# Optimization experiments

Hardware: AMD Instinct MI355X
Metric: run time of the kernel (lower is better)

Reference implementation:

```python
import jax, jax.numpy as jnp
import numpy as np

IN_CH = 256
HID = 64
HEADS = 3 * 0 + 4  # num_heads


def setup_inputs() -> dict:
    key = jax.random.key(0)
    ks = jax.random.split(key, 5)
    B, C, H, W = 2, IN_CH, 64, 64
    x = jax.random.normal(ks[0], (B, C, H, W), dtype=jnp.float32)
    # per-head embed conv (kernel 1 -> stored as [heads, 3*HID, C]); kaiming fan_out-ish scale
    w_embed = jax.random.normal(ks[1], (HEADS, 3 * HID, C), dtype=jnp.float32) * np.float32(np.sqrt(2.0 / (3 * HID)))
    b_embed = jnp.zeros((HEADS, 3 * HID), dtype=jnp.float32)
    # output ConvTranspose2d(hidden*heads -> C, kernel 1): weight [hidden*heads, C]
    w_out = jax.random.normal(ks[2], (HEADS * HID, C), dtype=jnp.float32) * np.float32(np.sqrt(2.0 / C))
    b_out = jnp.zeros((C,), dtype=jnp.float32)
    return {"x": x, "w_embed": w_embed, "b_embed": b_embed, "w_out": w_out, "b_out": b_out}


def reference(x, w_embed, b_embed, w_out, b_out):
    B, C, H, W = x.shape
    N = H * W
    nH = w_embed.shape[0]
    D = w_embed.shape[1] // 3
    scale = D ** -0.5
    # 1x1 embed conv per head: [B, nH, 3D, N]
    xf = x.reshape(B, C, N)
    qkv = jnp.einsum('bcn,hdc->bhdn', xf, w_embed) + b_embed[None, :, :, None]
    q, k, v = jnp.split(qkv, 3, axis=2)  # each [B, nH, D, N]
    attn = jnp.einsum('bhci,bhcj->bhij', q, k) * scale  # [B, nH, N, N]
    attn = jax.nn.softmax(attn, axis=-1)
    y = jnp.einsum('bhij,bhcj->bhci', attn, v)  # [B, nH, D, N]
    y = y.reshape(B, nH * D, N)
    # output 1x1 transposed conv (kernel 1 == plain 1x1 projection)
    out = jnp.einsum('bkn,kc->bcn', y, w_out) + b_out[None, :, None]
    out = out.reshape(B, C, H, W)
    return out + x  # residual
```

## Files before the change

kernel.cpp:

```cpp
#include <hip/hip_runtime.h>
#include <hip/hip_bf16.h>

#define NH   4
#define D_   64
#define N_   4096
#define C_   256
#define ME   768
#define QSCALE 0.18033688f

typedef float    f32x4  __attribute__((ext_vector_type(4)));
typedef float    f32x16 __attribute__((ext_vector_type(16)));
typedef _Float16 f16x8  __attribute__((ext_vector_type(8)));
typedef _Float16 f16x4  __attribute__((ext_vector_type(4)));

__global__ __launch_bounds__(256) void prep_kernel(const float* __restrict__ x,
                                                   const float* __restrict__ w_out,
                                                   _Float16* __restrict__ xT,
                                                   _Float16* __restrict__ w_outT) {
    __shared__ float T[64][68];
    const int t = threadIdx.x, bx = blockIdx.x;
    if (bx < 512) {
        const int n0 = (bx & 63) * 64, c0 = ((bx >> 6) & 3) * 64, b = bx >> 8;
        const float* xp = x + ((size_t)b * C_ + c0) * N_ + n0;
        #pragma unroll
        for (int r = 0; r < 4; ++r) {
            int idx = r * 256 + t;
            int c = idx >> 4, ng = (idx & 15) * 4;
            *(f32x4*)&T[c][ng] = *(const f32x4*)(xp + (size_t)c * N_ + ng);
        }
        __syncthreads();
        _Float16* dp = xT + ((size_t)b * N_ + n0) * C_ + c0;
        #pragma unroll
        for (int r = 0; r < 2; ++r) {
            int idx = r * 256 + t;
            int n = idx >> 3, cg = (idx & 7) * 8;
            f16x8 v;
            #pragma unroll
            for (int j = 0; j < 8; ++j) v[j] = (_Float16)T[cg + j][n];
            *(f16x8*)(dp + (size_t)n * C_ + cg) = v;
        }
    } else {
        int tile = bx - 512;
        int tc = tile & 3, tk = tile >> 2;
        #pragma unroll
        for (int r = 0; r < 4; ++r) {
            int idx = r * 256 + t;
            int kl = idx >> 4, cl = (idx & 15) * 4;
            *(f32x4*)&T[kl][cl] = *(const f32x4*)(w_out + (size_t)(tk * 64 + kl) * C_ + tc * 64 + cl);
        }
        __syncthreads();
        #pragma unroll
        for (int r = 0; r < 2; ++r) {
            int idx = r * 256 + t;
            int cl = idx >> 3, kg = (idx & 7) * 8;
            f16x8 v;
            #pragma unroll
            for (int j = 0; j < 8; ++j) v[j] = (_Float16)T[kg + j][cl];
            *(f16x8*)(w_outT + (size_t)(tc * 64 + cl) * C_ + tk * 64 + kg) = v;
        }
    }
}

__global__ __launch_bounds__(256) void qkv_gemm(const _Float16* __restrict__ xT,
                                                const float* __restrict__ w_embed,
                                                const float* __restrict__ b_embed,
                                                _Float16* __restrict__ qT,
                                                _Float16* __restrict__ kT,
                                                _Float16* __restrict__ vB) {
    __shared__ __align__(16) union SM {
        struct { _Float16 A[2][64][40], X[2][64][40]; } s;
        float Os[64][68];
    } sm;
    const int n0 = blockIdx.x * 64, mt = blockIdx.y, b = blockIdx.z;
    const int m0 = mt * 64;
    const int t = threadIdx.x;
    const int lane = t & 63, w = t >> 6, quad = lane >> 4, l16 = lane & 15;
    const int srow = t >> 2, skoff = (t & 3) * 8;
    const int h = mt / 3, r3 = mt - h * 3;
    const float oscale = (r3 == 0) ? QSCALE : 1.0f;
    const float* ap = w_embed + (size_t)(m0 + srow) * C_ + skoff;
    const _Float16* xp = xT + ((size_t)b * N_ + n0 + srow) * C_ + skoff;
    f32x4 a0pre = *(const f32x4*)(ap);
    f32x4 a1pre = *(const f32x4*)(ap + 4);
    f16x8 xpre  = *(const f16x8*)(xp);
    f32x4 acc[4] = {};
    int cur = 0;
    for (int k0 = 0; k0 < C_; k0 += 32, cur ^= 1) {
        {
            f16x8 av = { (_Float16)a0pre[0], (_Float16)a0pre[1], (_Float16)a0pre[2], (_Float16)a0pre[3],
                         (_Float16)a1pre[0], (_Float16)a1pre[1], (_Float16)a1pre[2], (_Float16)a1pre[3] };
            *(f16x8*)&sm.s.A[cur][srow][skoff] = av;
            *(f16x8*)&sm.s.X[cur][srow][skoff] = xpre;
        }
        __syncthreads();
        if (k0 + 32 < C_) {
            a0pre = *(const f32x4*)(ap + k0 + 32);
            a1pre = *(const f32x4*)(ap + k0 + 36);
            xpre  = *(const f16x8*)(xp + k0 + 32);
        }
        f16x8 af = *(const f16x8*)&sm.s.A[cur][w * 16 + l16][quad * 8];
        #pragma unroll
        for (int nb = 0; nb < 4; ++nb) {
            f16x8 bf = *(const f16x8*)&sm.s.X[cur][nb * 16 + l16][quad * 8];
            acc[nb] = __builtin_amdgcn_mfma_f32_16x16x32_f16(af, bf, acc[nb], 0, 0, 0);
        }
    }
    float bias[4];
    #pragma unroll
    for (int rg = 0; rg < 4; ++rg) bias[rg] = b_embed[m0 + w * 16 + quad * 4 + rg];
    __syncthreads();
    #pragma unroll
    for (int nb = 0; nb < 4; ++nb)
        #pragma unroll
        for (int rg = 0; rg < 4; ++rg)
            sm.Os[w * 16 + quad * 4 + rg][nb * 16 + l16] = (acc[nb][rg] + bias[rg]) * oscale;
    __syncthreads();
    const int bh = b * NH + h;
    if (r3 < 2) {
        _Float16* dst = (r3 ? kT : qT) + ((size_t)bh * N_ + n0) * D_;
        #pragma unroll
        for (int r = 0; r < 2; ++r) {
            int idx = r * 256 + t;
            int n = idx >> 3, mg = (idx & 7) * 8;
            f16x8 v;
            #pragma unroll
            for (int j = 0; j < 8; ++j) v[j] = (_Float16)sm.Os[mg + j][n];
            *(f16x8*)(dst + (size_t)n * D_ + mg) = v;
        }
    } else {
        _Float16* dst = vB + (size_t)bh * D_ * N_ + n0;
        #pragma unroll
        for (int r = 0; r < 2; ++r) {
            int idx = r * 256 + t;
            int d = idx >> 3, ng = (idx & 7) * 8;
            f32x4 a = *(const f32x4*)&sm.Os[d][ng];
            f32x4 b2 = *(const f32x4*)&sm.Os[d][ng + 4];
            f16x8 v = { (_Float16)a[0], (_Float16)a[1], (_Float16)a[2], (_Float16)a[3],
                        (_Float16)b2[0], (_Float16)b2[1], (_Float16)b2[2], (_Float16)b2[3] };
            *(f16x8*)(dst + (size_t)d * N_ + ng) = v;
        }
    }
}

__global__ __launch_bounds__(256, 4) void attn_kernel(const _Float16* __restrict__ qT,
                                                      const _Float16* __restrict__ kT,
                                                      const _Float16* __restrict__ vB,
                                                      _Float16* __restrict__ opart,
                                                      float* __restrict__ mpart,
                                                      float* __restrict__ lpart,
                                                      int splog) {
    __shared__ __align__(16) union SM {
        struct { _Float16 K[64][76], V[64][76]; } s;
        _Float16 Os[128][76];
    } sm;
    const int t = threadIdx.x;
    const int nsp = 1 << splog;
    const int qt = blockIdx.x, h = blockIdx.y;
    const int b = blockIdx.z >> splog, s = blockIdx.z & (nsp - 1);
    const int bh = b * NH + h, sbh = s * 8 + bh;
    const _Float16* kp = kT + (size_t)bh * N_ * D_;
    const _Float16* vp = vB + (size_t)bh * D_ * N_;
    const int lane = t & 63, w = t >> 6, l32 = lane & 31, hl = lane >> 5;
    const int srow = t >> 3, scol = (t & 7) * 8;

    const _Float16* qp = qT + ((size_t)bh * N_ + qt * 128 + w * 32 + l32) * D_;
    f16x8 qf[4];
    #pragma unroll
    for (int kc = 0; kc < 4; ++kc) qf[kc] = *(const f16x8*)(qp + kc * 16 + hl * 8);

    f32x16 oacc0 = {}, oacc1 = {};
    float m_run = 0.f, l_run = 0.f;

    const int niter = 64 >> splog;
    const int jt_lo = s * niter, jt_hi = jt_lo + niter;
    f16x8 kpre[2], vpre[2];
    #pragma unroll
    for (int r = 0; r < 2; ++r) {
        int row = srow + r * 32;
        kpre[r] = *(const f16x8*)(kp + (size_t)(jt_lo * 64 + row) * D_ + scol);
        vpre[r] = *(const f16x8*)(vp + (size_t)row * N_ + jt_lo * 64 + scol);
    }

    for (int jt = jt_lo; jt < jt_hi; ++jt) {
        __syncthreads();
        #pragma unroll
        for (int r = 0; r < 2; ++r) {
            int row = srow + r * 32;
            *(f16x8*)&sm.s.K[row][scol] = kpre[r];
            *(f16x8*)&sm.s.V[row][scol] = vpre[r];
        }
        __syncthreads();
        if (jt + 1 < jt_hi) {
            #pragma unroll
            for (int r = 0; r < 2; ++r) {
                int row = srow + r * 32;
                kpre[r] = *(const f16x8*)(kp + (size_t)((jt + 1) * 64 + row) * D_ + scol);
                vpre[r] = *(const f16x8*)(vp + (size_t)row * N_ + (jt + 1) * 64 + scol);
            }
        }
        f32x16 sa0 = {}, sa1 = {};
        #pragma unroll
        for (int kc = 0; kc < 4; ++kc) {
            f16x8 kf0 = *(const f16x8*)&sm.s.K[l32][kc * 16 + hl * 8];
            sa0 = __builtin_amdgcn_mfma_f32_32x32x16_f16(kf0, qf[kc], sa0, 0, 0, 0);
            f16x8 kf1 = *(const f16x8*)&sm.s.K[32 + l32][kc * 16 + hl * 8];
            sa1 = __builtin_amdgcn_mfma_f32_32x32x16_f16(kf1, qf[kc], sa1, 0, 0, 0);
        }
        if (jt == jt_lo) {
            f32x16 mm;
            #pragma unroll
            for (int r = 0; r < 16; ++r) mm[r] = fmaxf(sa0[r], sa1[r]);
            f32x4 m4;
            #pragma unroll
            for (int r = 0; r < 4; ++r)
                m4[r] = fmaxf(fmaxf(mm[r], mm[r + 4]), fmaxf(mm[r + 8], mm[r + 12]));
            float mx = fmaxf(fmaxf(m4[0], m4[1]), fmaxf(m4[2], m4[3]));
            mx = fmaxf(mx, __shfl_xor(mx, 32));
            m_run = mx + 8.0f;
        }
        #pragma unroll
        for (int r = 0; r < 16; ++r) sa0[r] = __builtin_amdgcn_exp2f(sa0[r] - m_run);
        #pragma unroll
        for (int r = 0; r < 16; ++r) sa1[r] = __builtin_amdgcn_exp2f(sa1[r] - m_run);
        f32x16 sv = sa0 + sa1;
        f32x4 s4;
        #pragma unroll
        for (int r = 0; r < 4; ++r) s4[r] = (sv[r] + sv[r + 4]) + (sv[r + 8] + sv[r + 12]);
        float rs = (s4[0] + s4[1]) + (s4[2] + s4[3]);
        rs += __shfl_xor(rs, 32);
        l_run += rs;
        #pragma unroll
        for (int jb = 0; jb < 2; ++jb) {
            const f32x16& sa = jb ? sa1 : sa0;
            union BU { f16x4 v; int d[2]; } bf[4];
            #pragma unroll
            for (int q = 0; q < 8; ++q)
                bf[q >> 1].d[q & 1] =
                    __builtin_bit_cast(int, __builtin_amdgcn_cvt_pkrtz(sa[2 * q], sa[2 * q + 1]));
            #pragma unroll
            for (int c = 0; c < 4; ++c) {
                const int vcol = jb * 32 + c * 8 + hl * 4;
                f16x4 va = *(const f16x4*)&sm.s.V[l32][vcol];
                oacc0 = __builtin_amdgcn_mfma_f32_32x32x8f16(va, bf[c].v, oacc0, 0, 0, 0);
                f16x4 vb = *(const f16x4*)&sm.s.V[32 + l32][vcol];
                oacc1 = __builtin_amdgcn_mfma_f32_32x32x8f16(vb, bf[c].v, oacc1, 0, 0, 0);
            }
        }
    }
    float linv = 1.f / l_run;
    if (hl == 0) {
        mpart[(size_t)sbh * N_ + qt * 128 + w * 32 + l32] = m_run;
        lpart[(size_t)sbh * N_ + qt * 128 + w * 32 + l32] = l_run;
    }
    __syncthreads();
    #pragma unroll
    for (int db = 0; db < 2; ++db) {
        const f32x16& oc = db ? oacc1 : oacc0;
        #pragma unroll
        for (int rq = 0; rq < 4; ++rq) {
            f16x4 pv = { (_Float16)(oc[rq * 4 + 0] * linv), (_Float16)(oc[rq * 4 + 1] * linv),
                         (_Float16)(oc[rq * 4 + 2] * linv), (_Float16)(oc[rq * 4 + 3] * linv) };
            *(f16x4*)&sm.Os[w * 32 + l32][db * 32 + rq * 8 + hl * 4] = pv;
        }
    }
    __syncthreads();
    _Float16* op = opart + ((size_t)sbh * N_ + qt * 128) * D_;
    #pragma unroll
    for (int r = 0; r < 4; ++r) {
        int idx = r * 256 + t;
        int i = idx >> 3, ch = (idx & 7) * 8;
        *(f16x8*)(op + (size_t)i * D_ + ch) = *(const f16x8*)&sm.Os[i][ch];
    }
}

__global__ __launch_bounds__(256) void projc_gemm(const _Float16* __restrict__ opart,
                                                  const float* __restrict__ mpart,
                                                  const float* __restrict__ lpart,
                                                  const _Float16* __restrict__ w_outT,
                                                  const float* __restrict__ b_out,
                                                  const float* __restrict__ x,
                                                  float* __restrict__ out) {
    __shared__ __align__(16) union SMP {
        struct {
            _Float16 Y[16][264];
            union { float W[4][16][4]; _Float16 A[128][40]; } u;
        } p;
        float Os[128][20];
    } sm;
    const int nt = blockIdx.x, chh = blockIdx.y, b = blockIdx.z;
    const int n0 = nt * 16, c0 = chh * 128;
    const int t = threadIdx.x;
    const int lane = t & 63, w = t >> 6, quad = lane >> 4, l16 = lane & 15;

    if (t < 64) {
        const int nl = t & 15, hh = t >> 4;
        const int bh = b * NH + hh;
        float mv[4], lv[4];
        #pragma unroll
        for (int sI = 0; sI < 4; ++sI) {
            mv[sI] = mpart[(size_t)(sI * 8 + bh) * N_ + n0 + nl];
            lv[sI] = lpart[(size_t)(sI * 8 + bh) * N_ + n0 + nl];
        }
        float M = fmaxf(fmaxf(mv[0], mv[1]), fmaxf(mv[2], mv[3]));
        float ws[4], sum = 0.f;
        #pragma unroll
        for (int sI = 0; sI < 4; ++sI) {
            ws[sI] = __builtin_amdgcn_exp2f(mv[sI] - M) * lv[sI];
            sum += ws[sI];
        }
        float inv = 1.f / sum;
        #pragma unroll
        for (int sI = 0; sI < 4; ++sI) sm.p.u.W[hh][nl][sI] = ws[sI] * inv;
    }
    __syncthreads();

    #pragma unroll
    for (int it = 0; it < 2; ++it) {
        int idx = it * 256 + t;
        int n = idx >> 5, kg = (idx & 31) * 8;
        int hh = kg >> 6, d0 = kg & 63;
        const int bh = b * NH + hh;
        const float* Wn = &sm.p.u.W[hh][n][0];
        float accf[8] = {};
        #pragma unroll
        for (int sI = 0; sI < 4; ++sI) {
            f16x8 ov = *(const f16x8*)(opart + ((size_t)(sI * 8 + bh) * N_ + n0 + n) * D_ + d0);
            float wsv = Wn[sI];
            #pragma unroll
            for (int j = 0; j < 8; ++j) accf[j] += wsv * (float)ov[j];
        }
        f16x8 yv;
        #pragma unroll
        for (int j = 0; j < 8; ++j) yv[j] = (_Float16)accf[j];
        *(f16x8*)&sm.p.Y[n][kg] = yv;
    }
    __syncthreads();

    const int srow = t >> 1, skoff = (t & 1) * 16;
    const _Float16* ap = w_outT + (size_t)(c0 + srow) * C_ + skoff;
    f16x8 apre0 = *(const f16x8*)(ap);
    f16x8 apre1 = *(const f16x8*)(ap + 8);
    f32x4 acc[2] = {};
    for (int k0 = 0; k0 < C_; k0 += 32) {
        __syncthreads();
        *(f16x8*)&sm.p.u.A[srow][skoff]     = apre0;
        *(f16x8*)&sm.p.u.A[srow][skoff + 8] = apre1;
        __syncthreads();
        if (k0 + 32 < C_) {
            apre0 = *(const f16x8*)(ap + k0 + 32);
            apre1 = *(const f16x8*)(ap + k0 + 40);
        }
        f16x8 bf = *(const f16x8*)&sm.p.Y[l16][k0 + quad * 8];
        #pragma unroll
        for (int cb = 0; cb < 2; ++cb) {
            f16x8 af = *(const f16x8*)&sm.p.u.A[w * 32 + cb * 16 + l16][quad * 8];
            acc[cb] = __builtin_amdgcn_mfma_f32_16x16x32_f16(af, bf, acc[cb], 0, 0, 0);
        }
    }
    __syncthreads();
    #pragma unroll
    for (int cb = 0; cb < 2; ++cb)
        #pragma unroll
        for (int rg = 0; rg < 4; ++rg)
            sm.Os[w * 32 + cb * 16 + quad * 4 + rg][l16] =
                acc[cb][rg] + b_out[c0 + w * 32 + cb * 16 + quad * 4 + rg];
    __syncthreads();
    const float* xp = x + ((size_t)b * C_ + c0) * N_ + n0;
    float* op = out + ((size_t)b * C_ + c0) * N_ + n0;
    #pragma unroll
    for (int r = 0; r < 2; ++r) {
        int idx = r * 256 + t;
        int c = idx >> 2, ng = (idx & 3) * 4;
        f32x4 v  = *(const f32x4*)&sm.Os[c][ng];
        f32x4 xv = *(const f32x4*)(xp + (size_t)c * N_ + ng);
        f32x4 o  = { v[0] + xv[0], v[1] + xv[1], v[2] + xv[2], v[3] + xv[3] };
        *(f32x4*)(op + (size_t)c * N_ + ng) = o;
    }
}

extern "C" void kernel_launch(void* const* d_in, const int* in_sizes, int n_in,
                              void* d_out, int out_size, void* d_ws, size_t ws_size,
                              hipStream_t stream) {
    const float* x       = (const float*)d_in[0];
    const float* w_embed = (const float*)d_in[1];
    const float* b_embed = (const float*)d_in[2];
    const float* w_out   = (const float*)d_in[3];
    const float* b_out   = (const float*)d_in[4];
    float* out = (float*)d_out;

    const int splog = 2;

    _Float16* base   = (_Float16*)d_ws;
    _Float16* xT     = base;
    _Float16* w_outT = base + 2293760;
    _Float16* qT     = base + 2359296;
    _Float16* kT     = base + 4456448;
    _Float16* vB     = base + 6553600;
    _Float16* opart  = base + 8650752;
    float*    mpart  = (float*)(opart + (size_t)4 * 8 * N_ * D_);
    float*    lpart  = mpart + (size_t)4 * 8 * N_;

    prep_kernel<<<dim3(528, 1, 1), 256, 0, stream>>>(x, w_out, xT, w_outT);
    qkv_gemm   <<<dim3(64, 12, 2), 256, 0, stream>>>(xT, w_embed, b_embed, qT, kT, vB);
    attn_kernel<<<dim3(32, 4, 2 << splog), 256, 0, stream>>>(qT, kT, vB, opart, mpart, lpart, splog);
    projc_gemm <<<dim3(256, 2, 2), 256, 0, stream>>>(opart, mpart, lpart, w_outT, b_out, x, out);
}
```

Before: 144.5 us.

## Remap attention blocks per XCD for L2 reuse and merge projection channel halves

The attention grid is flattened to 1D and block ids are remapped so that all 32 query tiles of one (batch, head, split) group land on the same XCD. Those blocks then share K/V tiles in that XCD's L2. The output projection now computes all 256 channels per block instead of splitting them across two blocks. This avoids recomputing the split-combine of partial attention outputs twice, at the cost of larger shared memory and less grid parallelism.

```diff
diff --git a/kernel.cpp b/kernel.cpp
--- a/kernel.cpp
+++ b/kernel.cpp
@@ -155,8 +155,12 @@
     } sm;
     const int t = threadIdx.x;
     const int nsp = 1 << splog;
-    const int qt = blockIdx.x, h = blockIdx.y;
-    const int b = blockIdx.z >> splog, s = blockIdx.z & (nsp - 1);
+    const int bid = blockIdx.x;
+    const int xcd = bid & 7, slot = bid >> 3;
+    const int qt = slot & 31;
+    const int g = xcd + 8 * (slot >> 5);
+    const int h = g & 3, bz = g >> 2;
+    const int b = bz >> splog, s = bz & (nsp - 1);
     const int bh = b * NH + h, sbh = s * 8 + bh;
     const _Float16* kp = kT + (size_t)bh * N_ * D_;
     const _Float16* vp = vB + (size_t)bh * D_ * N_;
@@ -283,12 +287,12 @@
     __shared__ __align__(16) union SMP {
         struct {
             _Float16 Y[16][264];
-            union { float W[4][16][4]; _Float16 A[128][40]; } u;
+            union { float W[4][16][4]; _Float16 A[256][40]; } u;
         } p;
-        float Os[128][20];
+        float Os[256][20];
     } sm;
-    const int nt = blockIdx.x, chh = blockIdx.y, b = blockIdx.z;
-    const int n0 = nt * 16, c0 = chh * 128;
+    const int nt = blockIdx.x, b = blockIdx.z;
+    const int n0 = nt * 16;
     const int t = threadIdx.x;
     const int lane = t & 63, w = t >> 6, quad = lane >> 4, l16 = lane & 15;
 
@@ -336,39 +340,44 @@
     }
     __syncthreads();
 
-    const int srow = t >> 1, skoff = (t & 1) * 16;
-    const _Float16* ap = w_outT + (size_t)(c0 + srow) * C_ + skoff;
+    const _Float16* ap = w_outT + (size_t)t * C_;
     f16x8 apre0 = *(const f16x8*)(ap);
     f16x8 apre1 = *(const f16x8*)(ap + 8);
-    f32x4 acc[2] = {};
+    f16x8 apre2 = *(const f16x8*)(ap + 16);
+    f16x8 apre3 = *(const f16x8*)(ap + 24);
+    f32x4 acc[4] = {};
     for (int k0 = 0; k0 < C_; k0 += 32) {
         __syncthreads();
-        *(f16x8*)&sm.p.u.A[srow][skoff]     = apre0;
-        *(f16x8*)&sm.p.u.A[srow][skoff + 8] = apre1;
+        *(f16x8*)&sm.p.u.A[t][0]  = apre0;
+        *(f16x8*)&sm.p.u.A[t][8]  = apre1;
+        *(f16x8*)&sm.p.u.A[t][16] = apre2;
+        *(f16x8*)&sm.p.u.A[t][24] = apre3;
         __syncthreads();
         if (k0 + 32 < C_) {
             apre0 = *(const f16x8*)(ap + k0 + 32);
             apre1 = *(const f16x8*)(ap + k0 + 40);
+            apre2 = *(const f16x8*)(ap + k0 + 48);
+            apre3 = *(const f16x8*)(ap + k0 + 56);
         }
         f16x8 bf = *(const f16x8*)&sm.p.Y[l16][k0 + quad * 8];
         #pragma unroll
-        for (int cb = 0; cb < 2; ++cb) {
-            f16x8 af = *(const f16x8*)&sm.p.u.A[w * 32 + cb * 16 + l16][quad * 8];
+        for (int cb = 0; cb < 4; ++cb) {
+            f16x8 af = *(const f16x8*)&sm.p.u.A[w * 64 + cb * 16 + l16][quad * 8];
             acc[cb] = __builtin_amdgcn_mfma_f32_16x16x32_f16(af, bf, acc[cb], 0, 0, 0);
         }
     }
     __syncthreads();
     #pragma unroll
-    for (int cb = 0; cb < 2; ++cb)
+    for (int cb = 0; cb < 4; ++cb)
         #pragma unroll
         for (int rg = 0; rg < 4; ++rg)
-            sm.Os[w * 32 + cb * 16 + quad * 4 + rg][l16] =
-                acc[cb][rg] + b_out[c0 + w * 32 + cb * 16 + quad * 4 + rg];
-    __syncthreads();
-    const float* xp = x + ((size_t)b * C_ + c0) * N_ + n0;
-    float* op = out + ((size_t)b * C_ + c0) * N_ + n0;
-    #pragma unroll
-    for (int r = 0; r < 2; ++r) {
+            sm.Os[w * 64 + cb * 16 + quad * 4 + rg][l16] =
+                acc[cb][rg] + b_out[w * 64 + cb * 16 + quad * 4 + rg];
+    __syncthreads();
+    const float* xp = x + (size_t)b * C_ * N_ + n0;
+    float* op = out + (size_t)b * C_ * N_ + n0;
+    #pragma unroll
+    for (int r = 0; r < 4; ++r) {
         int idx = r * 256 + t;
         int c = idx >> 2, ng = (idx & 3) * 4;
         f32x4 v  = *(const f32x4*)&sm.Os[c][ng];
@@ -402,6 +411,6 @@
 
     prep_kernel<<<dim3(528, 1, 1), 256, 0, stream>>>(x, w_out, xT, w_outT);
     qkv_gemm   <<<dim3(64, 12, 2), 256, 0, stream>>>(xT, w_embed, b_embed, qT, kT, vB);
-    attn_kernel<<<dim3(32, 4, 2 << splog), 256, 0, stream>>>(qT, kT, vB, opart, mpart, lpart, splog);
-    projc_gemm <<<dim3(256, 2, 2), 256, 0, stream>>>(opart, mpart, lpart, w_outT, b_out, x, out);
+    attn_kernel<<<dim3(1024, 1, 1), 256, 0, stream>>>(qT, kT, vB, opart, mpart, lpart, splog);
+    projc_gemm <<<dim3(256, 1, 2), 256, 0, stream>>>(opart, mpart, lpart, w_outT, b_out, x, out);
 }
```

After: 145.9 us. About the same (+1.0%).
